# Kernel optimization log

Hardware: AMD Instinct MI355X
Metric: run time of the kernel (lower is better)

The kernel has to match this reference:

```python
import jax, jax.numpy as jnp
import numpy as np

B, C, G, E, R, T, L, K = 8, 192, 256, 384, 4, 8192, 3, 3
DILATIONS = (1, 3, 9)
EPS = 1e-5


def setup_inputs() -> dict:
    key = jax.random.key(0)
    ks = jax.random.split(key, 16)
    s = 0.05
    return {
        'x': jax.random.normal(ks[0], (B, C, T), jnp.float32),
        'x_mask': jnp.ones((B, 1, T), jnp.float32),
        'g': jax.random.normal(ks[1], (B, G, 1), jnp.float32),
        'dconv_w': jax.random.normal(ks[2], (L, C, K), jnp.float32) * s,
        'dconv_b': jax.random.normal(ks[3], (L, C), jnp.float32) * s,
        'ln_gamma': jnp.ones((L, C), jnp.float32),
        'ln_beta': jnp.zeros((L, C), jnp.float32),
        'p1_w': jax.random.normal(ks[4], (L, E, C), jnp.float32) * s,
        'p1_b': jax.random.normal(ks[5], (L, E), jnp.float32) * s,
        'p1_ain_w': jax.random.normal(ks[6], (L, C * R, G), jnp.float32) * 0.01,
        'p1_ain_b': jnp.zeros((L, C * R), jnp.float32),
        'p1_aout_w': jax.random.normal(ks[7], (L, E * R, G), jnp.float32) * 0.01,
        'p1_aout_b': jnp.zeros((L, E * R), jnp.float32),
        'p2_w': jax.random.normal(ks[8], (L, C, E), jnp.float32) * s,
        'p2_b': jax.random.normal(ks[9], (L, C), jnp.float32) * s,
        'p2_ain_w': jax.random.normal(ks[10], (L, E * R, G), jnp.float32) * 0.01,
        'p2_ain_b': jnp.zeros((L, E * R), jnp.float32),
        'p2_aout_w': jax.random.normal(ks[11], (L, C * R, G), jnp.float32) * 0.01,
        'p2_aout_b': jnp.zeros((L, C * R), jnp.float32),
    }


def _causal_dconv(x, w, b, dilation):
    # x: [B,C,T]; w: [C,K] depthwise kernel; matches flip/pad/conv/flip in torch module
    xf = jnp.flip(x, 2)
    xf = jnp.pad(xf, ((0, 0), (0, 0), (0, (K - 1) * dilation)))
    y = jax.lax.conv_general_dilated(
        xf, w[:, None, :], window_strides=(1,), padding='VALID',
        rhs_dilation=(dilation,), dimension_numbers=('NCH', 'OIH', 'NCH'),
        feature_group_count=C)
    y = y + b[None, :, None]
    return jnp.flip(y, 2)


def _layernorm_c(x, gamma, beta):
    # LayerNorm over channel axis (axis=1)
    mu = jnp.mean(x, axis=1, keepdims=True)
    var = jnp.mean(jnp.square(x - mu), axis=1, keepdims=True)
    xn = (x - mu) * jax.lax.rsqrt(var + EPS)
    return xn * gamma[None, :, None] + beta[None, :, None]


def _lora(x, g2, w_main, b_main, ain_w, ain_b, aout_w, aout_b, cin, cout):
    # main 1x1 conv
    x_ = jnp.einsum('oc,bcl->bol', w_main, x) + b_main[None, :, None]
    a_in = (g2 @ ain_w.T + ain_b).reshape(-1, cin, R)      # [B,cin,R]
    a_out = (g2 @ aout_w.T + aout_b).reshape(-1, R, cout)  # [B,R,cout]
    t = jnp.einsum('bcl,bcr->brl', x, a_in)
    low = jnp.einsum('brl,brc->bcl', t, a_out)
    return x_ + low


def reference(x, x_mask, g, dconv_w, dconv_b, ln_gamma, ln_beta,
              p1_w, p1_b, p1_ain_w, p1_ain_b, p1_aout_w, p1_aout_b,
              p2_w, p2_b, p2_ain_w, p2_ain_b, p2_aout_w, p2_aout_b):
    g2 = g[:, :, 0]  # [B,G]
    x = x * x_mask
    for i in range(L):
        residual = x
        h = _causal_dconv(x, dconv_w[i], dconv_b[i], DILATIONS[i])
        h = _layernorm_c(h, ln_gamma[i], ln_beta[i])
        h = h * x_mask
        h = _lora(h, g2, p1_w[i], p1_b[i], p1_ain_w[i], p1_ain_b[i],
                  p1_aout_w[i], p1_aout_b[i], C, E)
        h = jax.nn.gelu(h, approximate=False)
        h = _lora(h, g2, p2_w[i], p2_b[i], p2_ain_w[i], p2_ain_b[i],
                  p2_aout_w[i], p2_aout_b[i], E, C)
        x = residual + h
    return x
```

## Files before the change

### kernel.cpp

```cpp
#include <hip/hip_runtime.h>
#include <hip/hip_bf16.h>

#define B_ 8
#define C_ 192
#define G_ 256
#define E_ 384
#define R_ 4
#define T_ 8192
#define L_ 3
#define K_ 3

typedef __attribute__((ext_vector_type(4))) float f32x4;
typedef __attribute__((ext_vector_type(8))) short bf16x8;
typedef __attribute__((ext_vector_type(4))) short bf16x4;

static __device__ __forceinline__ float bf2f(short u) {
    union { float f; unsigned int i; } z;
    z.i = ((unsigned int)(unsigned short)u) << 16;
    return z.f;
}

static __device__ __forceinline__ float gelu_fast(float x) {
    float x2 = x * x;
    float inner = fmaf(0.044715f * x, x2, x);
    float e = __expf(1.5957691216057308f * inner);
    float r = 1.0f / (e + 1.0f);
    float t = fmaf(-2.0f, r, 1.0f);
    float s = 0.5f * x;
    return fmaf(s, t, s);
}

__global__ __launch_bounds__(256) void adapters_kernel(
    const float* __restrict__ g2,
    const float* __restrict__ w0, const float* __restrict__ bi0, float* __restrict__ o0,
    const float* __restrict__ w1, const float* __restrict__ bi1, float* __restrict__ o1,
    const float* __restrict__ w2, const float* __restrict__ bi2, float* __restrict__ o2,
    const float* __restrict__ w3, const float* __restrict__ bi3, float* __restrict__ o3)
{
    const int N0 = L_ * B_ * (C_ * R_);
    const int N1 = L_ * B_ * (E_ * R_);
    int idx = blockIdx.x * 256 + threadIdx.x;
    const float* w; const float* bi; float* o; int rows; int li;
    if (idx < N0)                      { w=w0; bi=bi0; o=o0; rows=C_*R_; li=idx; }
    else if ((idx -= N0) < N1)         { w=w1; bi=bi1; o=o1; rows=E_*R_; li=idx; }
    else if ((idx -= N1) < N1)         { w=w2; bi=bi2; o=o2; rows=E_*R_; li=idx; }
    else if ((idx -= N1) < N0)         { w=w3; bi=bi3; o=o3; rows=C_*R_; li=idx; }
    else return;
    int bb = li & 7;
    int lr = li >> 3;
    const float4* wr = (const float4*)(w + (size_t)lr * G_);
    const float4* gb = (const float4*)(g2 + (size_t)bb * G_);
    float s = bi[lr];
#pragma unroll 8
    for (int g = 0; g < G_ / 4; ++g) {
        float4 a = gb[g], b = wr[g];
        s = fmaf(a.x, b.x, s); s = fmaf(a.y, b.y, s);
        s = fmaf(a.z, b.z, s); s = fmaf(a.w, b.w, s);
    }
    o[((size_t)(lr / rows) * B_ + bb) * rows + (lr % rows)] = s;
}

__global__ __launch_bounds__(256) void builds_kernel(
    const float* __restrict__ p1w, const float* __restrict__ p2w,
    const float* __restrict__ gam, const float* __restrict__ bet,
    const float* __restrict__ A1in, const float* __restrict__ A1out,
    const float* __restrict__ A2in, const float* __restrict__ A2out,
    __hip_bfloat16* __restrict__ W1, __hip_bfloat16* __restrict__ W2,
    float* __restrict__ C1)
{
    const int W1B = (L_ * B_ * E_ * C_) / 256;
    int blk = blockIdx.x;
    if (blk < W1B) {
        int idx = blk * 256 + threadIdx.x;
        int c = idx % C_;
        int e = (idx / C_) % E_;
        int b = (idx / (C_ * E_)) % B_;
        int l = idx / (C_ * E_ * B_);
        float v = p1w[((size_t)l * E_ + e) * C_ + c];
        const float* ai = A1in + ((size_t)l * B_ + b) * (C_ * R_);
        const float* ao = A1out + ((size_t)l * B_ + b) * (R_ * E_);
#pragma unroll
        for (int r = 0; r < R_; ++r) v = fmaf(ai[c * R_ + r], ao[r * E_ + e], v);
        W1[idx] = __float2bfloat16(v * gam[l * C_ + c]);
    } else if (blk < 2 * W1B) {
        int idx = (blk - W1B) * 256 + threadIdx.x;
        int e = idx % E_;
        int c = (idx / E_) % C_;
        int b = (idx / (C_ * E_)) % B_;
        int l = idx / (C_ * E_ * B_);
        float v = p2w[((size_t)l * C_ + c) * E_ + e];
        const float* ai = A2in + ((size_t)l * B_ + b) * (E_ * R_);
        const float* ao = A2out + ((size_t)l * B_ + b) * (R_ * C_);
#pragma unroll
        for (int r = 0; r < R_; ++r) v = fmaf(ai[e * R_ + r], ao[r * C_ + c], v);
        W2[idx] = __float2bfloat16(v);
    } else {
        int idx = (blk - 2 * W1B) * 256 + threadIdx.x;
        if (idx >= L_ * B_ * E_) return;
        int e = idx % E_;
        int b = (idx / E_) % B_;
        int l = idx / (E_ * B_);
        const float* wrow = p1w + ((size_t)l * E_ + e) * C_;
        const float* ai = A1in + ((size_t)l * B_ + b) * (C_ * R_);
        const float* ao = A1out + ((size_t)l * B_ + b) * (R_ * E_);
        const float* bt = bet + l * C_;
        float s = 0.f;
        for (int c = 0; c < C_; ++c) {
            float v = wrow[c];
#pragma unroll
            for (int r = 0; r < R_; ++r) v = fmaf(ai[c * R_ + r], ao[r * E_ + e], v);
            s = fmaf(v, bt[c], s);
        }
        C1[((size_t)l * B_ + b) * E_ + e] = s;
    }
}

__global__ __launch_bounds__(256) void transpose_in_kernel(
    const float* __restrict__ x, const float* __restrict__ mask,
    __hip_bfloat16* __restrict__ xw)
{
    __shared__ float tile[64][65];
    int b = blockIdx.z, c0 = blockIdx.y * 64, t0 = blockIdx.x * 64;
#pragma unroll
    for (int it = 0; it < 4; ++it) {
        int i = it * 256 + threadIdx.x;
        int r = i >> 4, cq = i & 15;
        float4 xv = *(const float4*)(&x[((size_t)b * C_ + c0 + r) * T_ + t0 + cq * 4]);
        float4 mv = *(const float4*)(&mask[(size_t)b * T_ + t0 + cq * 4]);
        tile[r][cq * 4 + 0] = xv.x * mv.x;
        tile[r][cq * 4 + 1] = xv.y * mv.y;
        tile[r][cq * 4 + 2] = xv.z * mv.z;
        tile[r][cq * 4 + 3] = xv.w * mv.w;
    }
    __syncthreads();
#pragma unroll
    for (int it = 0; it < 4; ++it) {
        int i = it * 256 + threadIdx.x;
        int r = i >> 4, cq = i & 15;
        union { __hip_bfloat16 h[4]; int2 i2; } u;
#pragma unroll
        for (int j = 0; j < 4; ++j) u.h[j] = __float2bfloat16(tile[cq * 4 + j][r]);
        *(int2*)(&xw[((size_t)b * T_ + t0 + r) * C_ + c0 + cq * 4]) = u.i2;
    }
}

__global__ __launch_bounds__(256) void transpose_out_kernel(
    const __hip_bfloat16* __restrict__ xw, float* __restrict__ out)
{
    __shared__ float tile[64][65];
    int b = blockIdx.z, c0 = blockIdx.y * 64, t0 = blockIdx.x * 64;
#pragma unroll
    for (int it = 0; it < 4; ++it) {
        int i = it * 256 + threadIdx.x;
        int r = i >> 4, cq = i & 15;
        bf16x4 v = *(const bf16x4*)(&xw[((size_t)b * T_ + t0 + r) * C_ + c0 + cq * 4]);
#pragma unroll
        for (int j = 0; j < 4; ++j) tile[cq * 4 + j][r] = bf2f(v[j]);
    }
    __syncthreads();
#pragma unroll
    for (int it = 0; it < 4; ++it) {
        int i = it * 256 + threadIdx.x;
        int r = i >> 4, cq = i & 15;
        float4 o;
        o.x = tile[r][cq * 4 + 0];
        o.y = tile[r][cq * 4 + 1];
        o.z = tile[r][cq * 4 + 2];
        o.w = tile[r][cq * 4 + 3];
        *(float4*)(&out[((size_t)b * C_ + c0 + r) * T_ + t0 + cq * 4]) = o;
    }
}

__global__ __launch_bounds__(256, 2) void ffn_fused_kernel(
    const __hip_bfloat16* __restrict__ xin, __hip_bfloat16* __restrict__ xout,
    const float* __restrict__ dw, const float* __restrict__ db,
    const float* __restrict__ mask,
    const __hip_bfloat16* __restrict__ W1, const float* __restrict__ b1,
    const float* __restrict__ c1,
    const __hip_bfloat16* __restrict__ W2, const float* __restrict__ b2,
    int dil)
{
    __shared__ __hip_bfloat16 Hs[64][C_ + 8];
    __shared__ __hip_bfloat16 H1s[64][E_ + 8];
    const int bid = blockIdx.x;
    const int b = bid & 7;
    const int t0 = (bid >> 3) * 64;
    const int tid = threadIdx.x;
    const int wv = tid >> 6, lane = tid & 63;
    const int llo = lane & 15, lhi = lane >> 4;
    const size_t xbase = (size_t)b * T_ * C_;

    {
        const int grp = tid >> 4, gl = tid & 15;
        const int cbase = gl * 12;
        float4 wf[9], dbf[3];
#pragma unroll
        for (int q = 0; q < 9; ++q) wf[q] = *(const float4*)(dw + cbase * 3 + q * 4);
#pragma unroll
        for (int q = 0; q < 3; ++q) dbf[q] = *(const float4*)(db + cbase + q * 4);
#pragma unroll
        for (int rr = 0; rr < 4; ++rr) {
            int tl = grp * 4 + rr;
            int t = t0 + tl;
            float v[12];
#pragma unroll
            for (int j = 0; j < 12; ++j) v[j] = ((const float*)dbf)[j];
#pragma unroll
            for (int k3 = 0; k3 < 3; ++k3) {
                int tt = t - k3 * dil;
                if (tt >= 0) {
                    const __hip_bfloat16* rp = xin + xbase + (size_t)tt * C_ + cbase;
#pragma unroll
                    for (int q = 0; q < 3; ++q) {
                        bf16x4 xv = *(const bf16x4*)(rp + q * 4);
#pragma unroll
                        for (int jj = 0; jj < 4; ++jj) {
                            int j = q * 4 + jj;
                            v[j] = fmaf(((const float*)wf)[j * 3 + k3], bf2f(xv[jj]), v[j]);
                        }
                    }
                }
            }
            float s = 0.f, sq = 0.f;
#pragma unroll
            for (int j = 0; j < 12; ++j) { s += v[j]; sq = fmaf(v[j], v[j], sq); }
#pragma unroll
            for (int o = 1; o <= 8; o <<= 1) {
                s += __shfl_xor(s, o, 64);
                sq += __shfl_xor(sq, o, 64);
            }
            float mu = s * (1.f / C_);
            float var = fmaf(sq, 1.f / C_, -mu * mu);
            float rs = rsqrtf(var + 1e-5f);
            float m = mask[(size_t)b * T_ + t];
            float sc = rs * m;
            float sh = -mu * sc;
            union { __hip_bfloat16 h[12]; int2 i2[3]; } u;
#pragma unroll
            for (int j = 0; j < 12; ++j)
                u.h[j] = __float2bfloat16(fmaf(v[j], sc, sh));
#pragma unroll
            for (int q = 0; q < 3; ++q)
                *(int2*)(&Hs[tl][cbase + q * 4]) = u.i2[q];
        }
    }
    __syncthreads();

    const __hip_bfloat16* w1p = W1 + (size_t)b * E_ * C_
        + (size_t)(wv * 96 + llo) * C_ + lhi * 8;
    f32x4 acc1[6][4] = {};
#pragma unroll
    for (int kc = 0; kc < 6; ++kc) {
        bf16x8 bfr[4];
#pragma unroll
        for (int nf = 0; nf < 4; ++nf)
            bfr[nf] = *(const bf16x8*)(&Hs[nf * 16 + llo][kc * 32 + lhi * 8]);
#pragma unroll
        for (int mf = 0; mf < 6; ++mf) {
            bf16x8 af = *(const bf16x8*)(w1p + (size_t)mf * 16 * C_ + kc * 32);
#pragma unroll
            for (int nf = 0; nf < 4; ++nf)
                acc1[mf][nf] = __builtin_amdgcn_mfma_f32_16x16x32_bf16(
                    af, bfr[nf], acc1[mf][nf], 0, 0, 0);
        }
    }

    float mcol[4];
#pragma unroll
    for (int nf = 0; nf < 4; ++nf)
        mcol[nf] = mask[(size_t)b * T_ + t0 + nf * 16 + llo];
#pragma unroll
    for (int mf = 0; mf < 6; ++mf) {
        int e0 = wv * 96 + mf * 16 + lhi * 4;
        float4 b1v = *(const float4*)(b1 + e0);
        float4 c1v = *(const float4*)(c1 + (size_t)b * E_ + e0);
#pragma unroll
        for (int nf = 0; nf < 4; ++nf) {
            union { __hip_bfloat16 h[4]; int2 i2; } u;
#pragma unroll
            for (int j = 0; j < 4; ++j) {
                float xx = acc1[mf][nf][j] + ((const float*)&b1v)[j]
                         + mcol[nf] * ((const float*)&c1v)[j];
                u.h[j] = __float2bfloat16(gelu_fast(xx));
            }
            *(int2*)(&H1s[nf * 16 + llo][e0]) = u.i2;
        }
    }
    __syncthreads();

    const __hip_bfloat16* w2p = W2 + (size_t)b * C_ * E_
        + (size_t)(wv * 48 + llo) * E_ + lhi * 8;
    f32x4 acc2[3][4] = {};
#pragma unroll
    for (int kc = 0; kc < 12; ++kc) {
        bf16x8 bfr[4];
#pragma unroll
        for (int nf = 0; nf < 4; ++nf)
            bfr[nf] = *(const bf16x8*)(&H1s[nf * 16 + llo][kc * 32 + lhi * 8]);
#pragma unroll
        for (int mf = 0; mf < 3; ++mf) {
            bf16x8 af = *(const bf16x8*)(w2p + (size_t)mf * 16 * E_ + kc * 32);
#pragma unroll
            for (int nf = 0; nf < 4; ++nf)
                acc2[mf][nf] = __builtin_amdgcn_mfma_f32_16x16x32_bf16(
                    af, bfr[nf], acc2[mf][nf], 0, 0, 0);
        }
    }

#pragma unroll
    for (int mf = 0; mf < 3; ++mf) {
        int c0 = wv * 48 + mf * 16 + lhi * 4;
        float4 b2v = *(const float4*)(b2 + c0);
#pragma unroll
        for (int nf = 0; nf < 4; ++nf) {
            int t = t0 + nf * 16 + llo;
            const __hip_bfloat16* pr = xin + xbase + (size_t)t * C_ + c0;
            __hip_bfloat16* po = xout + xbase + (size_t)t * C_ + c0;
            union { __hip_bfloat16 h[4]; int2 i2; } ui, uo;
            ui.i2 = *(const int2*)pr;
#pragma unroll
            for (int j = 0; j < 4; ++j)
                uo.h[j] = __float2bfloat16(
                    bf2f(*(short*)&ui.h[j]) + acc2[mf][nf][j] + ((const float*)&b2v)[j]);
            *(int2*)po = uo.i2;
        }
    }
}

extern "C" void kernel_launch(void* const* d_in, const int* in_sizes, int n_in,
                              void* d_out, int out_size, void* d_ws, size_t ws_size,
                              hipStream_t stream) {
    const float* x        = (const float*)d_in[0];
    const float* x_mask   = (const float*)d_in[1];
    const float* g        = (const float*)d_in[2];
    const float* dconv_w  = (const float*)d_in[3];
    const float* dconv_b  = (const float*)d_in[4];
    const float* ln_gamma = (const float*)d_in[5];
    const float* ln_beta  = (const float*)d_in[6];
    const float* p1_w     = (const float*)d_in[7];
    const float* p1_b     = (const float*)d_in[8];
    const float* p1_ain_w = (const float*)d_in[9];
    const float* p1_ain_b = (const float*)d_in[10];
    const float* p1_aout_w= (const float*)d_in[11];
    const float* p1_aout_b= (const float*)d_in[12];
    const float* p2_w     = (const float*)d_in[13];
    const float* p2_b     = (const float*)d_in[14];
    const float* p2_ain_w = (const float*)d_in[15];
    const float* p2_ain_b = (const float*)d_in[16];
    const float* p2_aout_w= (const float*)d_in[17];
    const float* p2_aout_b= (const float*)d_in[18];

    char* ws = (char*)d_ws;
    size_t off = 0;
    __hip_bfloat16* xwA = (__hip_bfloat16*)(ws + off); off += (size_t)B_ * T_ * C_ * 2;
    __hip_bfloat16* xwB = (__hip_bfloat16*)(ws + off); off += (size_t)B_ * T_ * C_ * 2;
    __hip_bfloat16* W1 = (__hip_bfloat16*)(ws + off);  off += (size_t)L_ * B_ * E_ * C_ * 2;
    __hip_bfloat16* W2 = (__hip_bfloat16*)(ws + off);  off += (size_t)L_ * B_ * C_ * E_ * 2;
    float* C1    = (float*)(ws + off); off += (size_t)L_ * B_ * E_ * 4;
    float* A1in  = (float*)(ws + off); off += (size_t)L_ * B_ * C_ * R_ * 4;
    float* A1out = (float*)(ws + off); off += (size_t)L_ * B_ * R_ * E_ * 4;
    float* A2in  = (float*)(ws + off); off += (size_t)L_ * B_ * E_ * R_ * 4;
    float* A2out = (float*)(ws + off); off += (size_t)L_ * B_ * R_ * C_ * 4;

    {
        int total = L_ * B_ * (2 * C_ * R_ + 2 * E_ * R_);
        adapters_kernel<<<(total + 255) / 256, 256, 0, stream>>>(
            g,
            p1_ain_w, p1_ain_b, A1in,
            p1_aout_w, p1_aout_b, A1out,
            p2_ain_w, p2_ain_b, A2in,
            p2_aout_w, p2_aout_b, A2out);
    }
    {
        int w1blocks = (L_ * B_ * E_ * C_) / 256;
        int c1blocks = (L_ * B_ * E_ + 255) / 256;
        builds_kernel<<<2 * w1blocks + c1blocks, 256, 0, stream>>>(
            p1_w, p2_w, ln_gamma, ln_beta,
            A1in, A1out, A2in, A2out, W1, W2, C1);
    }

    transpose_in_kernel<<<dim3(T_ / 64, C_ / 64, B_), 256, 0, stream>>>(x, x_mask, xwA);

    const int DILS[3] = {1, 3, 9};
    __hip_bfloat16* bufs[2] = {xwA, xwB};
    for (int l = 0; l < L_; ++l) {
        ffn_fused_kernel<<<(T_ / 64) * B_, 256, 0, stream>>>(
            bufs[l & 1], bufs[(l & 1) ^ 1],
            dconv_w + l * C_ * K_, dconv_b + l * C_, x_mask,
            W1 + (size_t)l * B_ * E_ * C_, p1_b + l * E_,
            C1 + (size_t)l * B_ * E_,
            W2 + (size_t)l * B_ * C_ * E_, p2_b + l * C_, DILS[l]);
    }

    transpose_out_kernel<<<dim3(T_ / 64, C_ / 64, B_), 256, 0, stream>>>(xwB, (float*)d_out);
}
```

Measured before the change: 255.1 us.

## Fuse output transpose into last layer, prefetch MFMA operands, apply LN affine in-kernel

The final layer's fused FFN kernel now writes the fp32 [B,C,T] output directly through a shared-memory transpose tile, so the separate transpose_out kernel and its bf16 round trip are gone. Both MFMA loops now preload weight fragments two K-steps ahead and LDS fragments one step ahead, hiding global and LDS latency behind the MFMAs. The LayerNorm gamma/beta are applied in the dconv stage instead of being folded into W1 and a C1 bias, which removes the C1 build work. The cost is more registers for the prefetch buffers, which could reduce occupancy or cause spills, plus a somewhat more complex epilogue.

Measured after the change: 231.8 us. 9.2% less time.

```diff
diff --git a/kernel.cpp b/kernel.cpp
--- a/kernel.cpp
+++ b/kernel.cpp
@@ -62,11 +62,9 @@
 
 __global__ __launch_bounds__(256) void builds_kernel(
     const float* __restrict__ p1w, const float* __restrict__ p2w,
-    const float* __restrict__ gam, const float* __restrict__ bet,
     const float* __restrict__ A1in, const float* __restrict__ A1out,
     const float* __restrict__ A2in, const float* __restrict__ A2out,
-    __hip_bfloat16* __restrict__ W1, __hip_bfloat16* __restrict__ W2,
-    float* __restrict__ C1)
+    __hip_bfloat16* __restrict__ W1, __hip_bfloat16* __restrict__ W2)
 {
     const int W1B = (L_ * B_ * E_ * C_) / 256;
     int blk = blockIdx.x;
@@ -81,8 +79,8 @@
         const float* ao = A1out + ((size_t)l * B_ + b) * (R_ * E_);
 #pragma unroll
         for (int r = 0; r < R_; ++r) v = fmaf(ai[c * R_ + r], ao[r * E_ + e], v);
-        W1[idx] = __float2bfloat16(v * gam[l * C_ + c]);
-    } else if (blk < 2 * W1B) {
+        W1[idx] = __float2bfloat16(v);
+    } else {
         int idx = (blk - W1B) * 256 + threadIdx.x;
         int e = idx % E_;
         int c = (idx / E_) % C_;
@@ -94,24 +92,6 @@
 #pragma unroll
         for (int r = 0; r < R_; ++r) v = fmaf(ai[e * R_ + r], ao[r * C_ + c], v);
         W2[idx] = __float2bfloat16(v);
-    } else {
-        int idx = (blk - 2 * W1B) * 256 + threadIdx.x;
-        if (idx >= L_ * B_ * E_) return;
-        int e = idx % E_;
-        int b = (idx / E_) % B_;
-        int l = idx / (E_ * B_);
-        const float* wrow = p1w + ((size_t)l * E_ + e) * C_;
-        const float* ai = A1in + ((size_t)l * B_ + b) * (C_ * R_);
-        const float* ao = A1out + ((size_t)l * B_ + b) * (R_ * E_);
-        const float* bt = bet + l * C_;
-        float s = 0.f;
-        for (int c = 0; c < C_; ++c) {
-            float v = wrow[c];
-#pragma unroll
-            for (int r = 0; r < R_; ++r) v = fmaf(ai[c * R_ + r], ao[r * E_ + e], v);
-            s = fmaf(v, bt[c], s);
-        }
-        C1[((size_t)l * B_ + b) * E_ + e] = s;
     }
 }
 
@@ -144,44 +124,20 @@
     }
 }
 
-__global__ __launch_bounds__(256) void transpose_out_kernel(
-    const __hip_bfloat16* __restrict__ xw, float* __restrict__ out)
-{
-    __shared__ float tile[64][65];
-    int b = blockIdx.z, c0 = blockIdx.y * 64, t0 = blockIdx.x * 64;
-#pragma unroll
-    for (int it = 0; it < 4; ++it) {
-        int i = it * 256 + threadIdx.x;
-        int r = i >> 4, cq = i & 15;
-        bf16x4 v = *(const bf16x4*)(&xw[((size_t)b * T_ + t0 + r) * C_ + c0 + cq * 4]);
-#pragma unroll
-        for (int j = 0; j < 4; ++j) tile[cq * 4 + j][r] = bf2f(v[j]);
-    }
-    __syncthreads();
-#pragma unroll
-    for (int it = 0; it < 4; ++it) {
-        int i = it * 256 + threadIdx.x;
-        int r = i >> 4, cq = i & 15;
-        float4 o;
-        o.x = tile[r][cq * 4 + 0];
-        o.y = tile[r][cq * 4 + 1];
-        o.z = tile[r][cq * 4 + 2];
-        o.w = tile[r][cq * 4 + 3];
-        *(float4*)(&out[((size_t)b * C_ + c0 + r) * T_ + t0 + cq * 4]) = o;
-    }
-}
-
 __global__ __launch_bounds__(256, 2) void ffn_fused_kernel(
     const __hip_bfloat16* __restrict__ xin, __hip_bfloat16* __restrict__ xout,
     const float* __restrict__ dw, const float* __restrict__ db,
+    const float* __restrict__ gamma, const float* __restrict__ beta,
     const float* __restrict__ mask,
     const __hip_bfloat16* __restrict__ W1, const float* __restrict__ b1,
-    const float* __restrict__ c1,
     const __hip_bfloat16* __restrict__ W2, const float* __restrict__ b2,
-    int dil)
+    int dil, float* __restrict__ outF)
 {
-    __shared__ __hip_bfloat16 Hs[64][C_ + 8];
-    __shared__ __hip_bfloat16 H1s[64][E_ + 8];
+    __shared__ __align__(16) char smem[75776];
+    __hip_bfloat16 (*Hs)[C_ + 8]  = (__hip_bfloat16 (*)[C_ + 8])smem;
+    __hip_bfloat16 (*H1s)[E_ + 8] = (__hip_bfloat16 (*)[E_ + 8])(smem + 25600);
+    float (*Tile)[68] = (float (*)[68])smem;
+
     const int bid = blockIdx.x;
     const int b = bid & 7;
     const int t0 = (bid >> 3) * 64;
@@ -193,11 +149,15 @@
     {
         const int grp = tid >> 4, gl = tid & 15;
         const int cbase = gl * 12;
-        float4 wf[9], dbf[3];
+        float4 wf[9], dbf[3], gaf[3], bef[3];
 #pragma unroll
         for (int q = 0; q < 9; ++q) wf[q] = *(const float4*)(dw + cbase * 3 + q * 4);
 #pragma unroll
-        for (int q = 0; q < 3; ++q) dbf[q] = *(const float4*)(db + cbase + q * 4);
+        for (int q = 0; q < 3; ++q) {
+            dbf[q] = *(const float4*)(db + cbase + q * 4);
+            gaf[q] = *(const float4*)(gamma + cbase + q * 4);
+            bef[q] = *(const float4*)(beta + cbase + q * 4);
+        }
 #pragma unroll
         for (int rr = 0; rr < 4; ++rr) {
             int tl = grp * 4 + rr;
@@ -233,12 +193,13 @@
             float var = fmaf(sq, 1.f / C_, -mu * mu);
             float rs = rsqrtf(var + 1e-5f);
             float m = mask[(size_t)b * T_ + t];
-            float sc = rs * m;
-            float sh = -mu * sc;
             union { __hip_bfloat16 h[12]; int2 i2[3]; } u;
 #pragma unroll
-            for (int j = 0; j < 12; ++j)
-                u.h[j] = __float2bfloat16(fmaf(v[j], sc, sh));
+            for (int j = 0; j < 12; ++j) {
+                float xn = (v[j] - mu) * rs;
+                u.h[j] = __float2bfloat16(
+                    fmaf(xn, ((const float*)gaf)[j], ((const float*)bef)[j]) * m);
+            }
 #pragma unroll
             for (int q = 0; q < 3; ++q)
                 *(int2*)(&Hs[tl][cbase + q * 4]) = u.i2[q];
@@ -249,38 +210,50 @@
     const __hip_bfloat16* w1p = W1 + (size_t)b * E_ * C_
         + (size_t)(wv * 96 + llo) * C_ + lhi * 8;
     f32x4 acc1[6][4] = {};
-#pragma unroll
-    for (int kc = 0; kc < 6; ++kc) {
-        bf16x8 bfr[4];
+    {
+        bf16x8 af[3][6], bfr[2][4];
+#pragma unroll
+        for (int mf = 0; mf < 6; ++mf) {
+            af[0][mf] = *(const bf16x8*)(w1p + (size_t)mf * 16 * C_);
+            af[1][mf] = *(const bf16x8*)(w1p + (size_t)mf * 16 * C_ + 32);
+        }
 #pragma unroll
         for (int nf = 0; nf < 4; ++nf)
-            bfr[nf] = *(const bf16x8*)(&Hs[nf * 16 + llo][kc * 32 + lhi * 8]);
-#pragma unroll
-        for (int mf = 0; mf < 6; ++mf) {
-            bf16x8 af = *(const bf16x8*)(w1p + (size_t)mf * 16 * C_ + kc * 32);
-#pragma unroll
-            for (int nf = 0; nf < 4; ++nf)
-                acc1[mf][nf] = __builtin_amdgcn_mfma_f32_16x16x32_bf16(
-                    af, bfr[nf], acc1[mf][nf], 0, 0, 0);
-        }
-    }
-
-    float mcol[4];
-#pragma unroll
-    for (int nf = 0; nf < 4; ++nf)
-        mcol[nf] = mask[(size_t)b * T_ + t0 + nf * 16 + llo];
+            bfr[0][nf] = *(const bf16x8*)(&Hs[nf * 16 + llo][lhi * 8]);
+#pragma unroll
+        for (int kc = 0; kc < 6; ++kc) {
+            const int cur = kc % 3;
+            const int pf  = (kc + 2) % 3;
+            const int bc  = kc & 1;
+            if (kc < 4) {
+#pragma unroll
+                for (int mf = 0; mf < 6; ++mf)
+                    af[pf][mf] = *(const bf16x8*)(w1p + (size_t)mf * 16 * C_ + (kc + 2) * 32);
+            }
+            if (kc < 5) {
+#pragma unroll
+                for (int nf = 0; nf < 4; ++nf)
+                    bfr[bc ^ 1][nf] = *(const bf16x8*)(&Hs[nf * 16 + llo][(kc + 1) * 32 + lhi * 8]);
+            }
+#pragma unroll
+            for (int mf = 0; mf < 6; ++mf)
+#pragma unroll
+                for (int nf = 0; nf < 4; ++nf)
+                    acc1[mf][nf] = __builtin_amdgcn_mfma_f32_16x16x32_bf16(
+                        af[cur][mf], bfr[bc][nf], acc1[mf][nf], 0, 0, 0);
+        }
+    }
+
 #pragma unroll
     for (int mf = 0; mf < 6; ++mf) {
         int e0 = wv * 96 + mf * 16 + lhi * 4;
         float4 b1v = *(const float4*)(b1 + e0);
-        float4 c1v = *(const float4*)(c1 + (size_t)b * E_ + e0);
 #pragma unroll
         for (int nf = 0; nf < 4; ++nf) {
             union { __hip_bfloat16 h[4]; int2 i2; } u;
 #pragma unroll
             for (int j = 0; j < 4; ++j) {
-                float xx = acc1[mf][nf][j] + ((const float*)&b1v)[j]
-                         + mcol[nf] * ((const float*)&c1v)[j];
+                float xx = acc1[mf][nf][j] + ((const float*)&b1v)[j];
                 u.h[j] = __float2bfloat16(gelu_fast(xx));
             }
             *(int2*)(&H1s[nf * 16 + llo][e0]) = u.i2;
@@ -291,38 +264,84 @@
     const __hip_bfloat16* w2p = W2 + (size_t)b * C_ * E_
         + (size_t)(wv * 48 + llo) * E_ + lhi * 8;
     f32x4 acc2[3][4] = {};
-#pragma unroll
-    for (int kc = 0; kc < 12; ++kc) {
-        bf16x8 bfr[4];
+    {
+        bf16x8 af[3][3], bfr[2][4];
+#pragma unroll
+        for (int mf = 0; mf < 3; ++mf) {
+            af[0][mf] = *(const bf16x8*)(w2p + (size_t)mf * 16 * E_);
+            af[1][mf] = *(const bf16x8*)(w2p + (size_t)mf * 16 * E_ + 32);
+        }
 #pragma unroll
         for (int nf = 0; nf < 4; ++nf)
-            bfr[nf] = *(const bf16x8*)(&H1s[nf * 16 + llo][kc * 32 + lhi * 8]);
+            bfr[0][nf] = *(const bf16x8*)(&H1s[nf * 16 + llo][lhi * 8]);
+#pragma unroll
+        for (int kc = 0; kc < 12; ++kc) {
+            const int cur = kc % 3;
+            const int pf  = (kc + 2) % 3;
+            const int bc  = kc & 1;
+            if (kc < 10) {
+#pragma unroll
+                for (int mf = 0; mf < 3; ++mf)
+                    af[pf][mf] = *(const bf16x8*)(w2p + (size_t)mf * 16 * E_ + (kc + 2) * 32);
+            }
+            if (kc < 11) {
+#pragma unroll
+                for (int nf = 0; nf < 4; ++nf)
+                    bfr[bc ^ 1][nf] = *(const bf16x8*)(&H1s[nf * 16 + llo][(kc + 1) * 32 + lhi * 8]);
+            }
+#pragma unroll
+            for (int mf = 0; mf < 3; ++mf)
+#pragma unroll
+                for (int nf = 0; nf < 4; ++nf)
+                    acc2[mf][nf] = __builtin_amdgcn_mfma_f32_16x16x32_bf16(
+                        af[cur][mf], bfr[bc][nf], acc2[mf][nf], 0, 0, 0);
+        }
+    }
+
+    if (outF == nullptr) {
 #pragma unroll
         for (int mf = 0; mf < 3; ++mf) {
-            bf16x8 af = *(const bf16x8*)(w2p + (size_t)mf * 16 * E_ + kc * 32);
-#pragma unroll
-            for (int nf = 0; nf < 4; ++nf)
-                acc2[mf][nf] = __builtin_amdgcn_mfma_f32_16x16x32_bf16(
-                    af, bfr[nf], acc2[mf][nf], 0, 0, 0);
-        }
-    }
-
-#pragma unroll
-    for (int mf = 0; mf < 3; ++mf) {
-        int c0 = wv * 48 + mf * 16 + lhi * 4;
-        float4 b2v = *(const float4*)(b2 + c0);
-#pragma unroll
-        for (int nf = 0; nf < 4; ++nf) {
-            int t = t0 + nf * 16 + llo;
-            const __hip_bfloat16* pr = xin + xbase + (size_t)t * C_ + c0;
-            __hip_bfloat16* po = xout + xbase + (size_t)t * C_ + c0;
-            union { __hip_bfloat16 h[4]; int2 i2; } ui, uo;
-            ui.i2 = *(const int2*)pr;
-#pragma unroll
-            for (int j = 0; j < 4; ++j)
-                uo.h[j] = __float2bfloat16(
-                    bf2f(*(short*)&ui.h[j]) + acc2[mf][nf][j] + ((const float*)&b2v)[j]);
-            *(int2*)po = uo.i2;
+            int c0 = wv * 48 + mf * 16 + lhi * 4;
+            float4 b2v = *(const float4*)(b2 + c0);
+#pragma unroll
+            for (int nf = 0; nf < 4; ++nf) {
+                int t = t0 + nf * 16 + llo;
+                const __hip_bfloat16* pr = xin + xbase + (size_t)t * C_ + c0;
+                __hip_bfloat16* po = xout + xbase + (size_t)t * C_ + c0;
+                union { __hip_bfloat16 h[4]; int2 i2; } ui, uo;
+                ui.i2 = *(const int2*)pr;
+#pragma unroll
+                for (int j = 0; j < 4; ++j)
+                    uo.h[j] = __float2bfloat16(
+                        bf2f(*(short*)&ui.h[j]) + acc2[mf][nf][j] + ((const float*)&b2v)[j]);
+                *(int2*)po = uo.i2;
+            }
+        }
+    } else {
+        __syncthreads();
+#pragma unroll
+        for (int mf = 0; mf < 3; ++mf) {
+            int c0 = wv * 48 + mf * 16 + lhi * 4;
+            float4 b2v = *(const float4*)(b2 + c0);
+#pragma unroll
+            for (int nf = 0; nf < 4; ++nf) {
+                int tl = nf * 16 + llo;
+                const __hip_bfloat16* pr = xin + xbase + (size_t)(t0 + tl) * C_ + c0;
+                union { __hip_bfloat16 h[4]; int2 i2; } ui;
+                ui.i2 = *(const int2*)pr;
+#pragma unroll
+                for (int j = 0; j < 4; ++j)
+                    Tile[c0 + j][tl] =
+                        bf2f(*(short*)&ui.h[j]) + acc2[mf][nf][j] + ((const float*)&b2v)[j];
+            }
+        }
+        __syncthreads();
+#pragma unroll
+        for (int it = 0; it < 12; ++it) {
+            int i = it * 256 + tid;
+            int r = i >> 4, tq = i & 15;
+            float4 o = *(const float4*)(&Tile[r][tq * 4]);
+            *(float4*)(&outF[((size_t)b * C_ + r) * T_ + t0 + tq * 4]) = o;
         }
     }
 }
@@ -356,7 +375,6 @@
     __hip_bfloat16* xwB = (__hip_bfloat16*)(ws + off); off += (size_t)B_ * T_ * C_ * 2;
     __hip_bfloat16* W1 = (__hip_bfloat16*)(ws + off);  off += (size_t)L_ * B_ * E_ * C_ * 2;
     __hip_bfloat16* W2 = (__hip_bfloat16*)(ws + off);  off += (size_t)L_ * B_ * C_ * E_ * 2;
-    float* C1    = (float*)(ws + off); off += (size_t)L_ * B_ * E_ * 4;
     float* A1in  = (float*)(ws + off); off += (size_t)L_ * B_ * C_ * R_ * 4;
     float* A1out = (float*)(ws + off); off += (size_t)L_ * B_ * R_ * E_ * 4;
     float* A2in  = (float*)(ws + off); off += (size_t)L_ * B_ * E_ * R_ * 4;
@@ -373,10 +391,8 @@
     }
     {
         int w1blocks = (L_ * B_ * E_ * C_) / 256;
-        int c1blocks = (L_ * B_ * E_ + 255) / 256;
-        builds_kernel<<<2 * w1blocks + c1blocks, 256, 0, stream>>>(
-            p1_w, p2_w, ln_gamma, ln_beta,
-            A1in, A1out, A2in, A2out, W1, W2, C1);
+        builds_kernel<<<2 * w1blocks, 256, 0, stream>>>(
+            p1_w, p2_w, A1in, A1out, A2in, A2out, W1, W2);
     }
 
     transpose_in_kernel<<<dim3(T_ / 64, C_ / 64, B_), 256, 0, stream>>>(x, x_mask, xwA);
@@ -384,13 +400,12 @@
     const int DILS[3] = {1, 3, 9};
     __hip_bfloat16* bufs[2] = {xwA, xwB};
     for (int l = 0; l < L_; ++l) {
+        float* outF = (l == L_ - 1) ? (float*)d_out : nullptr;
         ffn_fused_kernel<<<(T_ / 64) * B_, 256, 0, stream>>>(
             bufs[l & 1], bufs[(l & 1) ^ 1],
-            dconv_w + l * C_ * K_, dconv_b + l * C_, x_mask,
+            dconv_w + l * C_ * K_, dconv_b + l * C_,
+            ln_gamma + l * C_, ln_beta + l * C_, x_mask,
             W1 + (size_t)l * B_ * E_ * C_, p1_b + l * E_,
-            C1 + (size_t)l * B_ * E_,
-            W2 + (size_t)l * B_ * C_ * E_, p2_b + l * C_, DILS[l]);
-    }
-
-    transpose_out_kernel<<<dim3(T_ / 64, C_ / 64, B_), 256, 0, stream>>>(xwB, (float*)d_out);
-}
+            W2 + (size_t)l * B_ * C_ * E_, p2_b + l * C_, DILS[l], outF);
+    }
+}
```
